# Kernel optimization log

Hardware: AMD Instinct MI355X
Metric: run time of the kernel (lower is better)

The kernel has to match this reference:

```python
import jax, jax.numpy as jnp
import numpy as np

# ---- layer config (yolov3, layer_no=2) ----
STRIDE = 8
N_CLASSES = 80
IGNORE_TH = 0.7
ANCHORS_PX = np.array([[10,13],[16,30],[33,23],[30,61],[62,45],[59,119],[116,90],[156,198],[373,326]], np.float32)
ALL_ANCHORS = ANCHORS_PX / STRIDE          # [9,2] in grid units
ANCHOR_ID_LO, ANCHOR_ID_HI = 0, 2          # anchor_mask[2] = [0,1,2]
ANCHORS = ALL_ANCHORS[ANCHOR_ID_LO:ANCHOR_ID_HI+1]  # [3,2]
NA = 3
NC = N_CLASSES + 5

B, IN_CH, NG, NBOX = 16, 256, 76, 50


def _safe_log(p):
    # emulate torch BCE's log clamp at -100; eps stops 0*inf -> nan
    return jnp.maximum(jnp.log(jnp.maximum(p, 1e-12)), -100.0)


def _bce_sum(p, t, w=None):
    l = -(t * _safe_log(p) + (1.0 - t) * _safe_log(1.0 - p))
    if w is not None:
        l = l * w
    return l.sum()


def setup_inputs() -> dict:
    key = jax.random.key(0)
    k1, k2, k3, k4, k5 = jax.random.split(key, 5)
    xin = jax.random.normal(k1, (B, IN_CH, NG, NG), jnp.float32)
    cls = jax.random.randint(k2, (B, NBOX, 1), 0, N_CLASSES).astype(jnp.float32)
    cxy = jax.random.uniform(k3, (B, NBOX, 2), jnp.float32, 0.02, 0.98)
    wh = jax.random.uniform(k4, (B, NBOX, 2), jnp.float32, 0.02, 0.40)
    labels = jnp.concatenate([cls, cxy, wh], axis=-1)  # [B,N,5]
    W = jax.random.normal(k5, (NA * NC, IN_CH), jnp.float32) * 0.02  # 1x1 conv
    b = jnp.zeros((NA * NC,), jnp.float32)
    return {"xin": xin, "labels": labels, "W": W, "b": b}


def _yolo_loss(xin, labels, W, b):
    nB, _, nG, _ = xin.shape
    anchors = jnp.asarray(ANCHORS, xin.dtype)          # [3,2]
    all_anchors = jnp.asarray(ALL_ANCHORS, xin.dtype)  # [9,2]

    # 1x1 conv -> [B, A, G, G, C]
    x = jnp.einsum('bchw,oc->bohw', xin, W) + b[None, :, None, None]
    x = x.reshape(nB, NA, NC, nG, nG).transpose(0, 1, 3, 4, 2)

    xy = jax.nn.sigmoid(x[..., :2])
    wh = x[..., 2:4]
    conf_cls = jax.nn.sigmoid(x[..., 4:])  # [B,A,G,G,1+ncls]

    gy, gx = jnp.meshgrid(jnp.arange(nG, dtype=x.dtype), jnp.arange(nG, dtype=x.dtype), indexing='ij')
    pred_boxes = jnp.stack([
        xy[..., 0] + gx,
        xy[..., 1] + gy,
        jnp.exp(wh[..., 0]) * anchors[:, 0][None, :, None, None],
        jnp.exp(wh[..., 1]) * anchors[:, 1][None, :, None, None]], axis=-1)  # [B,A,G,G,4]

    # ---- ground truth ----
    valid = labels.sum(-1) > 0                     # [B,N]
    gt_cls = labels[..., 0].astype(jnp.int32)
    gt = labels[..., 1:] * nG                      # [B,N,4] cx,cy,w,h in grid units
    gt_x, gt_y, gt_w, gt_h = gt[..., 0], gt[..., 1], gt[..., 2], gt[..., 3]
    gi = jnp.floor(gt_x).astype(jnp.int32)
    gj = jnp.floor(gt_y).astype(jnp.int32)

    # best anchor per gt: wh-IoU vs all 9 anchors (centered at origin)
    inter_a = jnp.minimum(gt_w[..., None], all_anchors[:, 0]) * jnp.minimum(gt_h[..., None], all_anchors[:, 1])
    union_a = gt_w[..., None] * gt_h[..., None] + all_anchors[:, 0] * all_anchors[:, 1] - inter_a
    best = jnp.argmax(inter_a / union_a, axis=-1)  # [B,N]
    in_mask = (best >= ANCHOR_ID_LO) & (best <= ANCHOR_ID_HI)
    a = jnp.where(in_mask, best % 3, -1)           # [B,N]

    # all-pairs IoU: pred boxes vs gt boxes (ignore mask)
    pb = pred_boxes.reshape(nB, -1, 4)             # [B,M,4], M = A*G*G
    pa_area = pb[..., 2] * pb[..., 3]
    gt_area = gt_w * gt_h
    tl = jnp.maximum(pb[:, :, None, :2] - pb[:, :, None, 2:] / 2, gt[:, None, :, :2] - gt[:, None, :, 2:] / 2)
    br = jnp.minimum(pb[:, :, None, :2] + pb[:, :, None, 2:] / 2, gt[:, None, :, :2] + gt[:, None, :, 2:] / 2)
    inter = jnp.prod(br - tl, -1) * jnp.all(tl < br, -1)
    iou = inter / (pa_area[:, :, None] + gt_area[:, None, :] - inter)
    iou = jnp.where(valid[:, None, :], iou, 0.0)
    best_iou = iou.max(-1)                         # [B,M]
    has_boxes = valid.any(-1)
    obj_mask = jnp.where(has_boxes[:, None], best_iou <= IGNORE_TH, True).reshape(nB, NA, nG, nG)

    # ---- scatter target assignment ----
    assign = valid & (a >= 0)
    a_safe = jnp.clip(a, 0, NA - 1)
    aw = anchors[a_safe, 0]
    ah = anchors[a_safe, 1]
    tvec = jnp.concatenate([
        (gt_x - jnp.floor(gt_x))[..., None],
        (gt_y - jnp.floor(gt_y))[..., None],
        jnp.log(gt_w / aw + 1e-16)[..., None],
        jnp.log(gt_h / ah + 1e-16)[..., None],
        jnp.ones_like(gt_x)[..., None],
        jax.nn.one_hot(gt_cls, N_CLASSES, dtype=x.dtype)], axis=-1)  # [B,N,NC]
    sval = 2.0 - gt_w * gt_h / (nG * nG)

    bf = jnp.broadcast_to(jnp.arange(nB)[:, None], a.shape).reshape(-1)
    af = jnp.where(assign, a_safe, NA).reshape(-1)  # NA is OOB -> dropped
    jf = gj.reshape(-1)
    if_ = gi.reshape(-1)

    target = jnp.zeros((nB, NA, nG, nG, NC), x.dtype).at[bf, af, jf, if_].set(tvec.reshape(-1, NC), mode='drop')
    scale = jnp.zeros((nB, NA, nG, nG), x.dtype).at[bf, af, jf, if_].set(sval.reshape(-1), mode='drop')
    obj_mask = obj_mask.at[bf, af, jf, if_].set(True, mode='drop')
    noobj = jnp.zeros((nB, NA, nG, nG), bool).at[bf, af, jf, if_].set(True, mode='drop')

    # ---- losses ----
    nm = noobj.astype(x.dtype)[..., None]
    p_obj = conf_cls[..., 0] * obj_mask
    t_obj = target[..., 4] * obj_mask
    p_xy = xy * nm
    t_xy = target[..., :2] * nm
    p_wh = wh * nm
    t_wh = target[..., 2:4] * nm
    p_cls = conf_cls[..., 1:] * nm
    t_cls = target[..., 5:] * nm
    sc = scale[..., None]

    loss_xy = _bce_sum(p_xy, t_xy, sc)
    rs = jnp.sqrt(sc)
    loss_wh = 0.5 * jnp.sum((p_wh * rs - t_wh * rs) ** 2)
    loss_obj = _bce_sum(p_obj, t_obj)
    loss_cls = _bce_sum(p_cls, t_cls)
    loss = loss_xy + loss_wh + loss_obj + loss_cls
    return jnp.stack([loss, loss_xy, loss_wh, loss_obj, loss_cls])


def reference(xin, labels, W, b):
    return _yolo_loss(xin, labels, W, b)
```

## Files before the change

### kernel.cpp

```cpp
#include <hip/hip_runtime.h>
#include <math.h>

#define NB    16
#define NAg   3
#define NCg   85
#define NCLS  80
#define NGg   76
#define NSp   (NGg*NGg)
#define NCELL (NAg*NSp)
#define NBOX  50
#define INCH  256

#define ACC_OFF  0
#define WIN_OFF  32
#define PRED_OFF (32 + NB*NCELL*4)
#define GD_OFF   (PRED_OFF + NB*15*NSp*4)
#define GI_OFF   (GD_OFF + NB*NBOX*10*4)
#define WS_NEED  (GI_OFF + NB*NBOX*2*4)

__device__ __constant__ float c_AW[9] = {1.25f,2.0f,4.125f,3.75f,7.75f,7.375f,14.5f,19.5f,46.625f};
__device__ __constant__ float c_AH[9] = {1.625f,3.75f,2.875f,7.625f,5.625f,14.875f,11.25f,24.75f,40.75f};

__device__ __forceinline__ float safe_log(float p) {
    return fmaxf(logf(fmaxf(p, 1e-12f)), -100.0f);
}
__device__ __forceinline__ float sigm(float x) {
    return 1.0f / (1.0f + expf(-x));
}

__global__ __launch_bounds__(256) void k_gemm15(
    const float* __restrict__ xin, const float* __restrict__ W,
    const float* __restrict__ bias, float* __restrict__ pred)
{
    const int s  = blockIdx.x * 256 + threadIdx.x;
    const int b  = blockIdx.y;
    const bool act = (s < NSp);
    const int ss = act ? s : 0;

    float acc[15];
#pragma unroll
    for (int f = 0; f < 15; f++) acc[f] = 0.f;

    const float* xp = xin + ((size_t)b * INCH) * NSp + ss;
#pragma unroll 4
    for (int c = 0; c < INCH; c++) {
        float v = xp[(size_t)c * NSp];
#pragma unroll
        for (int f = 0; f < 15; f++) {
            const int row = (f / 5) * NCg + (f % 5);
            acc[f] += W[row * INCH + c] * v;
        }
    }
    if (!act) return;

    const float gx = (float)(s % NGg);
    const float gy = (float)(s / NGg);

#pragma unroll
    for (int a = 0; a < 3; a++) {
        float x0 = acc[a*5+0] + bias[a*NCg+0];
        float x1 = acc[a*5+1] + bias[a*NCg+1];
        float x2 = acc[a*5+2] + bias[a*NCg+2];
        float x3 = acc[a*5+3] + bias[a*NCg+3];
        float x4 = acc[a*5+4] + bias[a*NCg+4];
        float px = sigm(x0) + gx;
        float py = sigm(x1) + gy;
        float pw = expf(x2) * c_AW[a];
        float ph = expf(x3) * c_AH[a];
        float cf = sigm(x4);
        size_t base = (((size_t)b*3 + a)*5) * NSp + s;
        pred[base + 0*NSp] = px;
        pred[base + 1*NSp] = py;
        pred[base + 2*NSp] = pw;
        pred[base + 3*NSp] = ph;
        pred[base + 4*NSp] = cf;
    }
}

__global__ void k_labels(const float* __restrict__ labels,
                         float* __restrict__ gdata, int* __restrict__ gint,
                         int* __restrict__ win)
{
    int t = blockIdx.x * blockDim.x + threadIdx.x;
    if (t >= NB * NBOX) return;
    int b = t / NBOX, n = t % NBOX;

    const float* L = labels + (size_t)t * 5;
    float l0 = L[0], l1 = L[1], l2 = L[2], l3 = L[3], l4 = L[4];
    int valid = (l0 + l1 + l2 + l3 + l4) > 0.f;

    float gx = l1 * NGg, gy = l2 * NGg, gw = l3 * NGg, gh = l4 * NGg;

    int best = 0; float brr = -1.f;
#pragma unroll
    for (int k = 0; k < 9; k++) {
        float inter = fminf(gw, c_AW[k]) * fminf(gh, c_AH[k]);
        float uni   = gw*gh + c_AW[k]*c_AH[k] - inter;
        float r     = inter / uni;
        if (r > brr) { brr = r; best = k; }
    }
    int a = (best <= 2) ? best : -1;
    int assign = valid && (a >= 0);
    int a_safe = a < 0 ? 0 : (a > 2 ? 2 : a);

    float* gd = gdata + (size_t)t * 10;
    gd[0] = gx; gd[1] = gy; gd[2] = gw; gd[3] = gh;
    gd[4] = gx - floorf(gx);
    gd[5] = gy - floorf(gy);
    gd[6] = logf(gw / c_AW[a_safe] + 1e-16f);
    gd[7] = logf(gh / c_AH[a_safe] + 1e-16f);
    gd[8] = 2.f - gw * gh / (float)NSp;
    gd[9] = valid ? 1.f : 0.f;

    int gi = (int)floorf(gx), gj = (int)floorf(gy);
    int inb = (gi >= 0) && (gi < NGg) && (gj >= 0) && (gj < NGg);
    int cell = (assign && inb) ? (a * NSp + gj * NGg + gi) : -1;
    gint[t*2 + 0] = cell;
    gint[t*2 + 1] = (int)l0;

    if (cell >= 0) atomicMax(&win[b * NCELL + cell], n + 1);
}

__global__ __launch_bounds__(256) void k_obj(
    const float* __restrict__ pred, const float* __restrict__ gdata,
    const int* __restrict__ win, float* __restrict__ acc)
{
    __shared__ float sb[NBOX][5];
    __shared__ int sHas;
    __shared__ float red[256];

    const int b = blockIdx.y;
    const int tid = threadIdx.x;

    if (tid < NBOX) {
        const float* gd = gdata + ((size_t)b * NBOX + tid) * 10;
        sb[tid][0] = gd[0]; sb[tid][1] = gd[1];
        sb[tid][2] = gd[2]; sb[tid][3] = gd[3];
        sb[tid][4] = gd[9];
    }
    if (tid == 0) sHas = 0;
    __syncthreads();
    if (tid < NBOX && sb[tid][4] > 0.f) atomicOr(&sHas, 1);
    __syncthreads();

    const int cell = blockIdx.x * 256 + tid;
    float l = 0.f;
    if (cell < NCELL) {
        int a = cell / NSp, s = cell % NSp;
        size_t pb = (((size_t)b*3 + a)*5) * NSp + s;
        float px = pred[pb + 0*NSp], py = pred[pb + 1*NSp];
        float pw = pred[pb + 2*NSp], ph = pred[pb + 3*NSp];
        float cf = pred[pb + 4*NSp];
        float pa = pw * ph;
        float bi = 0.f;
        for (int n = 0; n < NBOX; n++) {
            if (sb[n][4] > 0.f) {
                float gx = sb[n][0], gy = sb[n][1], gw = sb[n][2], gh = sb[n][3];
                float tlx = fmaxf(px - pw*0.5f, gx - gw*0.5f);
                float tly = fmaxf(py - ph*0.5f, gy - gh*0.5f);
                float brx = fminf(px + pw*0.5f, gx + gw*0.5f);
                float bry = fminf(py + ph*0.5f, gy + gh*0.5f);
                float inter = ((tlx < brx) && (tly < bry)) ? (brx-tlx)*(bry-tly) : 0.f;
                float iou = inter / (pa + gw*gh - inter);
                bi = fmaxf(bi, iou);
            }
        }
        bool maskpre  = sHas ? (bi <= 0.7f) : true;
        bool assigned = win[b * NCELL + cell] > 0;
        if (maskpre || assigned) {
            float t = assigned ? 1.f : 0.f;
            l = -(t * safe_log(cf) + (1.f - t) * safe_log(1.f - cf));
        }
    }
    red[tid] = l;
    __syncthreads();
    for (int o = 128; o > 0; o >>= 1) {
        if (tid < o) red[tid] += red[tid + o];
        __syncthreads();
    }
    if (tid == 0) atomicAdd(&acc[2], red[0]);
}

__global__ __launch_bounds__(256) void k_assigned(
    const float* __restrict__ xin, const float* __restrict__ W,
    const float* __restrict__ bias, const float* __restrict__ gdata,
    const int* __restrict__ gint, const int* __restrict__ win,
    float* __restrict__ acc)
{
    const int t = blockIdx.x;
    const int b = t / NBOX, n = t % NBOX;
    const int cell = gint[t*2];
    if (cell < 0) return;
    if (win[b * NCELL + cell] != n + 1) return;

    const int a = cell / NSp, s = cell % NSp;
    const int o0 = a * NCg;
    const int tid = threadIdx.x;

    __shared__ float4 col4[64];
    __shared__ float  xsh[NCg];
    __shared__ float  sacc[3];

    ((float*)col4)[tid] = xin[((size_t)b * INCH + tid) * NSp + s];
    if (tid < 3) sacc[tid] = 0.f;
    __syncthreads();

    const int wid = tid >> 6, lane = tid & 63;
    for (int o = wid; o < NCg; o += 4) {
        const float4 wv = *(const float4*)&W[(size_t)(o0 + o) * INCH + lane * 4];
        const float4 cv = col4[lane];
        float p = wv.x*cv.x + wv.y*cv.y + wv.z*cv.z + wv.w*cv.w;
        for (int off = 32; off; off >>= 1) p += __shfl_down(p, off);
        if (lane == 0) xsh[o] = p + bias[o0 + o];
    }
    __syncthreads();

    if (tid < NCg) {
        const float* gd = gdata + (size_t)t * 10;
        const float sval = gd[8];
        const int gcls = gint[t*2 + 1];
        float val = xsh[tid];
        float term; int slot;
        if (tid < 2) {
            float tgt = gd[4 + tid];
            float p = sigm(val);
            term = -(tgt * safe_log(p) + (1.f - tgt) * safe_log(1.f - p)) * sval;
            slot = 0;
        } else if (tid < 4) {
            float tgt = gd[4 + tid];
            float d = val - tgt;
            term = 0.5f * sval * d * d;
            slot = 1;
        } else if (tid == 4) {
            term = 0.f; slot = 2;
        } else {
            float tgt = ((tid - 5) == gcls) ? 1.f : 0.f;
            float p = sigm(val);
            term = -(tgt * safe_log(p) + (1.f - tgt) * safe_log(1.f - p));
            slot = 2;
        }
        atomicAdd(&sacc[slot], term);
    }
    __syncthreads();
    if (tid == 0) {
        atomicAdd(&acc[0], sacc[0]);
        atomicAdd(&acc[1], sacc[1]);
        atomicAdd(&acc[3], sacc[2]);
    }
}

__global__ void k_final(const float* __restrict__ acc, float* __restrict__ out)
{
    float xy = acc[0], wh = acc[1], ob = acc[2], cl = acc[3];
    out[0] = xy + wh + ob + cl;
    out[1] = xy; out[2] = wh; out[3] = ob; out[4] = cl;
}

extern "C" void kernel_launch(void* const* d_in, const int* in_sizes, int n_in,
                              void* d_out, int out_size, void* d_ws, size_t ws_size,
                              hipStream_t stream)
{
    const float* xin    = (const float*)d_in[0];
    const float* labels = (const float*)d_in[1];
    const float* W      = (const float*)d_in[2];
    const float* bias   = (const float*)d_in[3];

    char* ws = (char*)d_ws;
    float* acc   = (float*)(ws + ACC_OFF);
    int*   win   = (int*)  (ws + WIN_OFF);
    float* pred  = (float*)(ws + PRED_OFF);
    float* gdata = (float*)(ws + GD_OFF);
    int*   gint  = (int*)  (ws + GI_OFF);
    float* out   = (float*)d_out;

    hipMemsetAsync(ws, 0, PRED_OFF, stream);

    k_gemm15 <<<dim3((NSp + 255)/256, NB), 256, 0, stream>>>(xin, W, bias, pred);
    k_labels <<<dim3((NB*NBOX + 255)/256), 256, 0, stream>>>(labels, gdata, gint, win);
    k_obj    <<<dim3((NCELL + 255)/256, NB), 256, 0, stream>>>(pred, gdata, win, acc);
    k_assigned<<<dim3(NB*NBOX), 256, 0, stream>>>(xin, W, bias, gdata, gint, win, acc);
    k_final  <<<1, 1, 0, stream>>>(acc, out);
}
```

Before: 223.4 us.

## Split channel reduction across slices with float4 spatial vectors, fuse decode into obj kernel

The 15-output 1x1-conv GEMM now splits the 256 input channels into 4 slices across blockIdx.z, and each thread handles 4 spatial positions via float4 loads. The kernel writes raw partial sums. The obj kernel sums those partials, adds bias and applies the sigmoid/exp box decode itself. The goal is more parallelism and wider memory accesses over the large xin read, which was previously covered by only about 23x16 blocks. The cost is extra workspace and partial-sum traffic, plus a fallback path used when the workspace is too small.

Measured after the change: 203.3 us. -9.0%, faster.

```diff
diff --git a/kernel.cpp b/kernel.cpp
--- a/kernel.cpp
+++ b/kernel.cpp
@@ -13,10 +13,13 @@
 
 #define ACC_OFF  0
 #define WIN_OFF  32
-#define PRED_OFF (32 + NB*NCELL*4)
-#define GD_OFF   (PRED_OFF + NB*15*NSp*4)
+#define GD_OFF   (WIN_OFF + NB*NCELL*4)
 #define GI_OFF   (GD_OFF + NB*NBOX*10*4)
-#define WS_NEED  (GI_OFF + NB*NBOX*2*4)
+#define PART_OFF (GI_OFF + NB*NBOX*2*4)
+#define PART_SZ1 ((size_t)NB*15*NSp*4)
+#define NEED4    (PART_OFF + 4*PART_SZ1)
+#define NEED1    (PART_OFF + 1*PART_SZ1)
+#define ZERO_BYTES GD_OFF
 
 __device__ __constant__ float c_AW[9] = {1.25f,2.0f,4.125f,3.75f,7.75f,7.375f,14.5f,19.5f,46.625f};
 __device__ __constant__ float c_AH[9] = {1.625f,3.75f,2.875f,7.625f,5.625f,14.875f,11.25f,24.75f,40.75f};
@@ -28,53 +31,38 @@
     return 1.0f / (1.0f + expf(-x));
 }
 
-__global__ __launch_bounds__(256) void k_gemm15(
+template<int NSLICE>
+__global__ __launch_bounds__(256) void k_gemm_part(
     const float* __restrict__ xin, const float* __restrict__ W,
-    const float* __restrict__ bias, float* __restrict__ pred)
-{
-    const int s  = blockIdx.x * 256 + threadIdx.x;
+    float* __restrict__ part)
+{
+    constexpr int CPS = INCH / NSLICE;
+    const int g  = blockIdx.x * 256 + threadIdx.x;
+    if (g >= NSp/4) return;
     const int b  = blockIdx.y;
-    const bool act = (s < NSp);
-    const int ss = act ? s : 0;
-
-    float acc[15];
-#pragma unroll
-    for (int f = 0; f < 15; f++) acc[f] = 0.f;
-
-    const float* xp = xin + ((size_t)b * INCH) * NSp + ss;
-#pragma unroll 4
-    for (int c = 0; c < INCH; c++) {
-        float v = xp[(size_t)c * NSp];
+    const int sl = blockIdx.z;
+    const int s0 = g * 4;
+
+    float4 acc[15];
+#pragma unroll
+    for (int f = 0; f < 15; f++) acc[f] = make_float4(0.f,0.f,0.f,0.f);
+
+    const float* xp = xin + ((size_t)b * INCH + sl * CPS) * NSp + s0;
+    const float* wp = W + sl * CPS;
+#pragma unroll 8
+    for (int c = 0; c < CPS; c++) {
+        const float4 v = *(const float4*)(xp + (size_t)c * NSp);
 #pragma unroll
         for (int f = 0; f < 15; f++) {
             const int row = (f / 5) * NCg + (f % 5);
-            acc[f] += W[row * INCH + c] * v;
-        }
-    }
-    if (!act) return;
-
-    const float gx = (float)(s % NGg);
-    const float gy = (float)(s / NGg);
-
-#pragma unroll
-    for (int a = 0; a < 3; a++) {
-        float x0 = acc[a*5+0] + bias[a*NCg+0];
-        float x1 = acc[a*5+1] + bias[a*NCg+1];
-        float x2 = acc[a*5+2] + bias[a*NCg+2];
-        float x3 = acc[a*5+3] + bias[a*NCg+3];
-        float x4 = acc[a*5+4] + bias[a*NCg+4];
-        float px = sigm(x0) + gx;
-        float py = sigm(x1) + gy;
-        float pw = expf(x2) * c_AW[a];
-        float ph = expf(x3) * c_AH[a];
-        float cf = sigm(x4);
-        size_t base = (((size_t)b*3 + a)*5) * NSp + s;
-        pred[base + 0*NSp] = px;
-        pred[base + 1*NSp] = py;
-        pred[base + 2*NSp] = pw;
-        pred[base + 3*NSp] = ph;
-        pred[base + 4*NSp] = cf;
-    }
+            const float w = wp[row * INCH + c];
+            acc[f].x += w * v.x; acc[f].y += w * v.y;
+            acc[f].z += w * v.z; acc[f].w += w * v.w;
+        }
+    }
+#pragma unroll
+    for (int f = 0; f < 15; f++)
+        *(float4*)&part[(((size_t)sl * NB + b) * 15 + f) * NSp + s0] = acc[f];
 }
 
 __global__ void k_labels(const float* __restrict__ labels,
@@ -121,9 +109,11 @@
     if (cell >= 0) atomicMax(&win[b * NCELL + cell], n + 1);
 }
 
-__global__ __launch_bounds__(256) void k_obj(
-    const float* __restrict__ pred, const float* __restrict__ gdata,
-    const int* __restrict__ win, float* __restrict__ acc)
+template<int NSLICE>
+__global__ __launch_bounds__(256) void k_fuse(
+    const float* __restrict__ part, const float* __restrict__ bias,
+    const float* __restrict__ gdata, const int* __restrict__ win,
+    float* __restrict__ acc)
 {
     __shared__ float sb[NBOX][5];
     __shared__ int sHas;
@@ -146,11 +136,21 @@
     const int cell = blockIdx.x * 256 + tid;
     float l = 0.f;
     if (cell < NCELL) {
-        int a = cell / NSp, s = cell % NSp;
-        size_t pb = (((size_t)b*3 + a)*5) * NSp + s;
-        float px = pred[pb + 0*NSp], py = pred[pb + 1*NSp];
-        float pw = pred[pb + 2*NSp], ph = pred[pb + 3*NSp];
-        float cf = pred[pb + 4*NSp];
+        const int a = cell / NSp, s = cell % NSp;
+        float x0 = 0.f, x1 = 0.f, x2 = 0.f, x3 = 0.f, x4 = 0.f;
+#pragma unroll
+        for (int sl = 0; sl < NSLICE; sl++) {
+            const float* pp = part + (((size_t)sl * NB + b) * 15 + a * 5) * NSp + s;
+            x0 += pp[0*NSp]; x1 += pp[1*NSp]; x2 += pp[2*NSp];
+            x3 += pp[3*NSp]; x4 += pp[4*NSp];
+        }
+        const float gxf = (float)(s % NGg);
+        const float gyf = (float)(s / NGg);
+        float px = sigm(x0 + bias[a*NCg+0]) + gxf;
+        float py = sigm(x1 + bias[a*NCg+1]) + gyf;
+        float pw = expf(x2 + bias[a*NCg+2]) * c_AW[a];
+        float ph = expf(x3 + bias[a*NCg+3]) * c_AH[a];
+        float cf = sigm(x4 + bias[a*NCg+4]);
         float pa = pw * ph;
         float bi = 0.f;
         for (int n = 0; n < NBOX; n++) {
@@ -268,16 +268,25 @@
     char* ws = (char*)d_ws;
     float* acc   = (float*)(ws + ACC_OFF);
     int*   win   = (int*)  (ws + WIN_OFF);
-    float* pred  = (float*)(ws + PRED_OFF);
     float* gdata = (float*)(ws + GD_OFF);
     int*   gint  = (int*)  (ws + GI_OFF);
+    float* part  = (float*)(ws + PART_OFF);
     float* out   = (float*)d_out;
 
-    hipMemsetAsync(ws, 0, PRED_OFF, stream);
-
-    k_gemm15 <<<dim3((NSp + 255)/256, NB), 256, 0, stream>>>(xin, W, bias, pred);
-    k_labels <<<dim3((NB*NBOX + 255)/256), 256, 0, stream>>>(labels, gdata, gint, win);
-    k_obj    <<<dim3((NCELL + 255)/256, NB), 256, 0, stream>>>(pred, gdata, win, acc);
+    const bool big = (ws_size >= (size_t)NEED4);
+
+    hipMemsetAsync(ws, 0, ZERO_BYTES, stream);
+
+    k_labels<<<dim3((NB*NBOX + 255)/256), 256, 0, stream>>>(labels, gdata, gint, win);
+
+    const int gx = (NSp/4 + 255) / 256;
+    if (big) k_gemm_part<4><<<dim3(gx, NB, 4), 256, 0, stream>>>(xin, W, part);
+    else     k_gemm_part<1><<<dim3(gx, NB, 1), 256, 0, stream>>>(xin, W, part);
+
+    const int fx = (NCELL + 255) / 256;
+    if (big) k_fuse<4><<<dim3(fx, NB), 256, 0, stream>>>(part, bias, gdata, win, acc);
+    else     k_fuse<1><<<dim3(fx, NB), 256, 0, stream>>>(part, bias, gdata, win, acc);
+
     k_assigned<<<dim3(NB*NBOX), 256, 0, stream>>>(xin, W, bias, gdata, gint, win, acc);
-    k_final  <<<1, 1, 0, stream>>>(acc, out);
-}
+    k_final<<<1, 1, 0, stream>>>(acc, out);
+}
```
